# Kernel optimization log

Measured on AMD Instinct MI355X. Metric: run time of the kernel, lower is better.

The kernel has to match this reference:

```python
import jax, jax.numpy as jnp
import numpy as np

N = 16384      # nodes
E = 131072     # edges
L = 256        # latent size
H = 256        # mlp hidden size
S = 4          # message passing steps
OUT = 128      # decoder node output size
EPS = 1e-6     # flax LayerNorm epsilon


def _mlp(x, W0, b0, W1, b1):
    h = jax.nn.relu(x @ W0 + b0)
    return h @ W1 + b1


def _mlp_ln(x, W0, b0, W1, b1, ls, lb):
    y = _mlp(x, W0, b0, W1, b1)
    mu = y.mean(-1, keepdims=True)
    var = ((y - mu) ** 2).mean(-1, keepdims=True)
    return (y - mu) * jax.lax.rsqrt(var + EPS) * ls + lb


def setup_inputs() -> dict:
    key = jax.random.key(0)
    ks = iter(jax.random.split(key, 64))
    std = 0.02

    def w(shape):
        return jax.random.normal(next(ks), shape, dtype=jnp.float32) * std

    inp = {
        'node_feats': jax.random.normal(next(ks), (N, 3), dtype=jnp.float32),
        'edge_feats': jax.random.normal(next(ks), (E, 4), dtype=jnp.float32),
        'senders': jax.random.randint(next(ks), (E,), 0, N, dtype=jnp.int32),
        'receivers': jax.random.randint(next(ks), (E,), 0, N, dtype=jnp.int32),
        # node embedder MLP (3 -> H -> L) + LayerNorm
        'en_W0': w((3, H)), 'en_b0': jnp.zeros((H,)), 'en_W1': w((H, L)), 'en_b1': jnp.zeros((L,)),
        'en_ls': jnp.ones((L,)), 'en_lb': jnp.zeros((L,)),
        # edge embedder MLP (4 -> H -> L) + LayerNorm
        'ee_W0': w((4, H)), 'ee_b0': jnp.zeros((H,)), 'ee_W1': w((H, L)), 'ee_b1': jnp.zeros((L,)),
        'ee_ls': jnp.ones((L,)), 'ee_lb': jnp.zeros((L,)),
        # processor edge MLPs, stacked over S steps (3L -> H -> L) + LN
        'pe_W0': w((S, 3 * L, H)), 'pe_b0': jnp.zeros((S, H)), 'pe_W1': w((S, H, L)), 'pe_b1': jnp.zeros((S, L)),
        'pe_ls': jnp.ones((S, L)), 'pe_lb': jnp.zeros((S, L)),
        # processor node MLPs, stacked over S steps (2L -> H -> L) + LN
        'pn_W0': w((S, 2 * L, H)), 'pn_b0': jnp.zeros((S, H)), 'pn_W1': w((S, H, L)), 'pn_b1': jnp.zeros((S, L)),
        'pn_ls': jnp.ones((S, L)), 'pn_lb': jnp.zeros((S, L)),
        # node decoder MLP (L -> H -> OUT), no LayerNorm
        'dn_W0': w((L, H)), 'dn_b0': jnp.zeros((H,)), 'dn_W1': w((H, OUT)), 'dn_b1': jnp.zeros((OUT,)),
    }
    return inp


def reference(node_feats, edge_feats, senders, receivers,
              en_W0, en_b0, en_W1, en_b1, en_ls, en_lb,
              ee_W0, ee_b0, ee_W1, ee_b1, ee_ls, ee_lb,
              pe_W0, pe_b0, pe_W1, pe_b1, pe_ls, pe_lb,
              pn_W0, pn_b0, pn_W1, pn_b1, pn_ls, pn_lb,
              dn_W0, dn_b0, dn_W1, dn_b1):
    # Embed raw node/edge features into latent space.
    nodes = _mlp_ln(node_feats, en_W0, en_b0, en_W1, en_b1, en_ls, en_lb)   # [N, L]
    edges = _mlp_ln(edge_feats, ee_W0, ee_b0, ee_W1, ee_b1, ee_ls, ee_lb)   # [E, L]

    def step(carry, p):
        nodes, edges = carry
        (eW0, eb0, eW1, eb1, els, elb, nW0, nb0, nW1, nb1, nls, nlb) = p
        # Edge update: MLP on [edge, sender_node, receiver_node].
        ein = jnp.concatenate([edges, nodes[senders], nodes[receivers]], axis=-1)  # [E, 3L]
        new_e = _mlp_ln(ein, eW0, eb0, eW1, eb1, els, elb)                          # [E, L]
        # Aggregate new edge messages into receiver nodes (segment_sum).
        agg = jax.ops.segment_sum(new_e, receivers, num_segments=N)                # [N, L]
        # Node update: MLP on [node, aggregated messages].
        nin = jnp.concatenate([nodes, agg], axis=-1)                                # [N, 2L]
        new_n = _mlp_ln(nin, nW0, nb0, nW1, nb1, nls, nlb)                          # [N, L]
        # Residual connections (as in DeepTypedGraphNet processor).
        return (nodes + new_n, edges + new_e), None

    (nodes, edges), _ = jax.lax.scan(
        step, (nodes, edges),
        (pe_W0, pe_b0, pe_W1, pe_b1, pe_ls, pe_lb,
         pn_W0, pn_b0, pn_W1, pn_b1, pn_ls, pn_lb))

    # Decoder on nodes (no LayerNorm on the output head).
    out = _mlp(nodes, dn_W0, dn_b0, dn_W1, dn_b1)  # [N, OUT]
    return out
```

## Files before the change

### kernel.cpp

```cpp
#include <hip/hip_runtime.h>
#include <hip/hip_bf16.h>

#define NN 16384
#define NE 131072
#define L 256
#define SSTEPS 4
#define OUTD 128

typedef __attribute__((ext_vector_type(8))) short bf16x8;
typedef __attribute__((ext_vector_type(4))) float f32x4;

typedef const unsigned __attribute__((address_space(1)))* as1_u32p;
typedef unsigned __attribute__((address_space(3)))* as3_u32p;

__device__ __forceinline__ void gload16(const void* g, void* lds) {
  __builtin_amdgcn_global_load_lds((as1_u32p)g, (as3_u32p)lds, 16, 0, 0);
}

__device__ __forceinline__ short f2bs(float f) {
  unsigned u = __builtin_bit_cast(unsigned, f);
  u = (u + 0x7fffu + ((u >> 16) & 1u)) >> 16;
  return (short)u;
}
__device__ __forceinline__ float bs2f(short s) {
  unsigned u = ((unsigned)(unsigned short)s) << 16;
  return __builtin_bit_cast(float, u);
}
__device__ __forceinline__ unsigned cvt_pk_bf16(float lo, float hi) {
  unsigned r;
  asm("v_cvt_pk_bf16_f32 %0, %1, %2" : "=v"(r) : "v"(lo), "v"(hi));
  return r;
}
__device__ __forceinline__ bf16x8 pack_bf16x8(const float v[8]) {
  union { unsigned u[4]; bf16x8 b; } r;
#pragma unroll
  for (int k = 0; k < 4; ++k) r.u[k] = cvt_pk_bf16(v[2 * k], v[2 * k + 1]);
  return r.b;
}

__device__ __forceinline__ void store_tile(short* hs, int l, int mi, int nb,
                                           f32x4 v) {
  const int lm = l & 15, g = l >> 4;
#pragma unroll
  for (int i = 0; i < 4; ++i) {
    const float part = __shfl_xor(v[i], 1);
    if ((l & 1) == 0) {
      const int row = mi * 16 + g * 4 + i;
      const int col = nb + lm;
      const int off = (row * 512 + col * 2) ^ ((row & 7) << 4);
      *(unsigned*)((char*)hs + off) = cvt_pk_bf16(v[i], part);
    }
  }
}

template <int MI, int NT, int KC, int AST>
__device__ __forceinline__ void gemm_lds(const short* __restrict__ Wp,
                                         int Ncols, const short* hs, int n0,
                                         int l, f32x4 acc[MI][NT]) {
  const int lm = l & 15, g = l >> 4;
#pragma unroll
  for (int kc = 0; kc < KC; ++kc) {
    bf16x8 a[MI];
#pragma unroll
    for (int mi = 0; mi < MI; ++mi) {
      const int row = mi * 16 + lm;
      const int off = (row * AST + kc * 64 + g * 16) ^ ((row & 7) << 4);
      a[mi] = *(const bf16x8*)((const char*)hs + off);
    }
#pragma unroll
    for (int ni = 0; ni < NT; ++ni) {
      const int n = n0 + ni * 16 + lm;
      bf16x8 b = *(const bf16x8*)(Wp + ((size_t)kc * Ncols + n) * 32 + g * 8);
#pragma unroll
      for (int mi = 0; mi < MI; ++mi)
        acc[mi][ni] =
            __builtin_amdgcn_mfma_f32_16x16x32_bf16(a[mi], b, acc[mi][ni], 0, 0, 0);
    }
  }
}

__global__ void pack_w(const float* __restrict__ src, short* __restrict__ dst,
                       int K, int N, int cnt) {
  const size_t total = (size_t)K * N * cnt;
  for (size_t i = (size_t)blockIdx.x * blockDim.x + threadIdx.x; i < total;
       i += (size_t)gridDim.x * blockDim.x) {
    const size_t mat = i / ((size_t)K * N);
    const int rem = (int)(i - mat * (size_t)K * N);
    const int k = rem / N, n = rem - k * N;
    dst[mat * (size_t)K * N + ((size_t)(k >> 5) * N + n) * 32 + (k & 31)] =
        f2bs(src[i]);
  }
}

__global__ void pack_w0_pad(const float* __restrict__ src,
                            short* __restrict__ dst, int Kreal) {
  const int i = blockIdx.x * 256 + threadIdx.x;
  if (i >= 256 * 32) return;
  const int n = i >> 5, k = i & 31;
  dst[n * 32 + k] = (k < Kreal) ? f2bs(src[k * 256 + n]) : (short)0;
}

__device__ __forceinline__ void stage_tile256(const short* __restrict__ src0,
                                              short* As, int w, int l) {
#pragma unroll
  for (int i = 0; i < 4; ++i) {
    const int rbase = w * 8 + i * 2;
    const int r = rbase + (l >> 5);
    const int boff = ((l & 31) * 16) ^ ((r & 7) << 4);
    gload16((const char*)(src0 + (size_t)r * L) + boff, As + rbase * 256);
  }
}

__device__ __forceinline__ void stage_nodes_half16(
    const short* __restrict__ a_src, short* As, int w, int l, int n0) {
#pragma unroll
  for (int i = 0; i < 4; ++i) {
    const int r = w * 4 + i;
    if (l < 32) {
      const int cb = (l * 16) ^ ((r & 7) << 4);
      gload16((const char*)(a_src + (size_t)(n0 + r) * L) + cb, As + r * 512);
    }
  }
}

__global__ void csr_hist(const int* __restrict__ recv, int* __restrict__ deg) {
  const int e = blockIdx.x * 256 + threadIdx.x;
  atomicAdd(&deg[recv[e]], 1);
}
__global__ __launch_bounds__(256) void csr_scan(const int* __restrict__ deg,
                                                int* __restrict__ start,
                                                int* __restrict__ cursor) {
  __shared__ int part[256];
  const int t = threadIdx.x;
  int s = 0;
  for (int i = 0; i < NN / 256; ++i) s += deg[t * (NN / 256) + i];
  part[t] = s;
  __syncthreads();
  if (t == 0) {
    int acc = 0;
    for (int i = 0; i < 256; ++i) {
      const int v = part[i];
      part[i] = acc;
      acc += v;
    }
  }
  __syncthreads();
  int acc = part[t];
  for (int i = 0; i < NN / 256; ++i) {
    const int n = t * (NN / 256) + i;
    start[n] = acc;
    cursor[n] = acc;
    acc += deg[n];
  }
  if (t == 255) start[NN] = acc;
}
__global__ void csr_scatter(const int* __restrict__ recv,
                            int* __restrict__ cursor, int* __restrict__ elist) {
  const int e = blockIdx.x * 256 + threadIdx.x;
  const int p = atomicAdd(&cursor[recv[e]], 1);
  elist[p] = e;
}
__global__ void csr_sort(const int* __restrict__ start, int* __restrict__ elist) {
  const int n = blockIdx.x * blockDim.x + threadIdx.x;
  if (n >= NN) return;
  const int b = start[n], e = start[n + 1];
  for (int i = b + 1; i < e; ++i) {
    const int v = elist[i];
    int j = i - 1;
    while (j >= b && elist[j] > v) {
      elist[j + 1] = elist[j];
      --j;
    }
    elist[j + 1] = v;
  }
}
__global__ void permute_se(const int* __restrict__ elist,
                           const int* __restrict__ senders,
                           const int* __restrict__ receivers,
                           int* __restrict__ sn_p, int* __restrict__ rc_p) {
  const int p = blockIdx.x * 256 + threadIdx.x;
  const int e = elist[p];
  sn_p[p] = senders[e];
  rc_p[p] = receivers[e];
}

__device__ __forceinline__ void ln_row(const short* smem, int row, int seg,
                                       const float lsv[16], const float lbv[16],
                                       float ne[16]) {
  const int off0 = (row * 512 + seg * 16) ^ ((row & 7) << 4);
  const int off1 = (row * 512 + 256 + seg * 16) ^ ((row & 7) << 4);
  const bf16x8 y0 = *(const bf16x8*)((const char*)smem + off0);
  const bf16x8 y1 = *(const bf16x8*)((const char*)smem + off1);
  float v[16];
#pragma unroll
  for (int k = 0; k < 8; ++k) {
    v[k] = bs2f(y0[k]);
    v[8 + k] = bs2f(y1[k]);
  }
  float s = 0.f;
#pragma unroll
  for (int k = 0; k < 16; ++k) s += v[k];
#pragma unroll
  for (int o = 1; o < 16; o <<= 1) s += __shfl_xor(s, o);
  const float mu = s * (1.f / 256.f);
  float sq = 0.f;
#pragma unroll
  for (int k = 0; k < 16; ++k) {
    const float d = v[k] - mu;
    sq += d * d;
  }
#pragma unroll
  for (int o = 1; o < 16; o <<= 1) sq += __shfl_xor(sq, o);
  const float rstd = rsqrtf(sq * (1.f / 256.f) + 1e-6f);
#pragma unroll
  for (int k = 0; k < 16; ++k) ne[k] = (v[k] - mu) * rstd * lsv[k] + lbv[k];
}

__device__ __forceinline__ void load16(const float* __restrict__ p, int seg,
                                       float d[16]) {
  const float4 a0 = *(const float4*)(p + seg * 8);
  const float4 a1 = *(const float4*)(p + seg * 8 + 4);
  const float4 a2 = *(const float4*)(p + 128 + seg * 8);
  const float4 a3 = *(const float4*)(p + 128 + seg * 8 + 4);
  d[0] = a0.x; d[1] = a0.y; d[2] = a0.z; d[3] = a0.w;
  d[4] = a1.x; d[5] = a1.y; d[6] = a1.z; d[7] = a1.w;
  d[8] = a2.x; d[9] = a2.y; d[10] = a2.z; d[11] = a2.w;
  d[12] = a3.x; d[13] = a3.y; d[14] = a3.z; d[15] = a3.w;
}

__global__ __launch_bounds__(256, 4) void proj_mfma(
    const short* __restrict__ nodes_b, const short* __restrict__ Wfull,
    short* __restrict__ NSb, short* __restrict__ NRb) {
  __shared__ char smem[16384];
  short* As = (short*)smem;
  const int t = threadIdx.x, w = t >> 6, l = t & 63;
  const int tr = t >> 4, seg = t & 15;
  const int n0 = blockIdx.x * 32;
  const short* Wp = Wfull + (size_t)(8 + blockIdx.y * 8) * 256 * 32;
  short* out = blockIdx.y ? NRb : NSb;

  stage_tile256(nodes_b + (size_t)n0 * L, As, w, l);
  __syncthreads();

  f32x4 acc[2][4] = {};
  gemm_lds<2, 4, 8, 512>(Wp, L, As, w * 64, l, acc);
  __syncthreads();
#pragma unroll
  for (int ni = 0; ni < 4; ++ni)
#pragma unroll
    for (int mi = 0; mi < 2; ++mi)
      store_tile(As, l, mi, w * 64 + ni * 16, acc[mi][ni]);
  __syncthreads();

#pragma unroll
  for (int p = 0; p < 2; ++p) {
    const int row = p * 16 + tr;
    const int off0 = (row * 512 + seg * 16) ^ ((row & 7) << 4);
    const int off1 = (row * 512 + 256 + seg * 16) ^ ((row & 7) << 4);
    *(bf16x8*)(out + (size_t)(n0 + row) * L + seg * 8) =
        *(const bf16x8*)((const char*)As + off0);
    *(bf16x8*)(out + (size_t)(n0 + row) * L + 128 + seg * 8) =
        *(const bf16x8*)((const char*)As + off1);
  }
}

__global__ __launch_bounds__(256, 4) void edge_step_mfma(
    const short* __restrict__ NSb, const short* __restrict__ NRb,
    short* __restrict__ edges_b, short* __restrict__ new_e,
    const int* __restrict__ senders, const int* __restrict__ receivers,
    const short* __restrict__ W0p, const float* __restrict__ b0,
    const short* __restrict__ W1p, const float* __restrict__ b1,
    const float* __restrict__ ls, const float* __restrict__ lb) {
  __shared__ char smem[32768];
  short* As = (short*)smem;
  short* nsrB = (short*)(smem + 16384);
  const int t = threadIdx.x, w = t >> 6, l = t & 63;
  const int lm = l & 15, g = l >> 4;
  const int tr = t >> 4, seg = t & 15;
  const int e0 = blockIdx.x * 32;

  const int sn0 = senders[e0 + tr], rc0 = receivers[e0 + tr];
  const int sn1 = senders[e0 + 16 + tr], rc1 = receivers[e0 + 16 + tr];
  stage_tile256(edges_b + (size_t)e0 * L, As, w, l);
  __syncthreads();

  bf16x8 gn[2][2], gr[2][2];
  {
    const short* p0 = NSb + (size_t)sn0 * L + seg * 8;
    gn[0][0] = *(const bf16x8*)p0;
    gn[0][1] = *(const bf16x8*)(p0 + 128);
    const short* p1 = NSb + (size_t)sn1 * L + seg * 8;
    gn[1][0] = *(const bf16x8*)p1;
    gn[1][1] = *(const bf16x8*)(p1 + 128);
    const short* q0 = NRb + (size_t)rc0 * L + seg * 8;
    gr[0][0] = *(const bf16x8*)q0;
    gr[0][1] = *(const bf16x8*)(q0 + 128);
    const short* q1 = NRb + (size_t)rc1 * L + seg * 8;
    gr[1][0] = *(const bf16x8*)q1;
    gr[1][1] = *(const bf16x8*)(q1 + 128);
  }

  f32x4 acc[2][4] = {};
  gemm_lds<2, 4, 8, 512>(W0p, L, As, w * 64, l, acc);

  bf16x8 old0[2], old1[2];
#pragma unroll
  for (int p = 0; p < 2; ++p) {
    const int row = p * 16 + tr;
    old0[p] = *(const bf16x8*)((const char*)As +
                               ((row * 512 + seg * 16) ^ ((row & 7) << 4)));
    old1[p] = *(const bf16x8*)((const char*)As +
                               ((row * 512 + 256 + seg * 16) ^ ((row & 7) << 4)));
  }

#pragma unroll
  for (int p = 0; p < 2; ++p) {
    const int row = p * 16 + tr;
    float s[16];
#pragma unroll
    for (int k = 0; k < 8; ++k) {
      s[k] = bs2f(gn[p][0][k]) + bs2f(gr[p][0][k]);
      s[8 + k] = bs2f(gn[p][1][k]) + bs2f(gr[p][1][k]);
    }
    const int off0 = (row * 512 + seg * 16) ^ ((row & 7) << 4);
    const int off1 = (row * 512 + 256 + seg * 16) ^ ((row & 7) << 4);
    *(bf16x8*)((char*)nsrB + off0) = pack_bf16x8(s);
    *(bf16x8*)((char*)nsrB + off1) = pack_bf16x8(s + 8);
  }
  __syncthreads();

#pragma unroll
  for (int ni = 0; ni < 4; ++ni) {
    const float bia = b0[w * 64 + ni * 16 + lm];
    const int col = w * 64 + ni * 16 + lm;
#pragma unroll
    for (int mi = 0; mi < 2; ++mi) {
      f32x4 v = acc[mi][ni];
#pragma unroll
      for (int i = 0; i < 4; ++i) {
        const int row = mi * 16 + g * 4 + i;
        const int noff = (row * 512 + col * 2) ^ ((row & 7) << 4);
        v[i] = fmaxf(v[i] + bia + bs2f(*(const short*)((const char*)nsrB + noff)),
                     0.f);
      }
      store_tile(As, l, mi, w * 64 + ni * 16, v);
    }
  }
  __syncthreads();

  f32x4 acc2[2][4] = {};
  gemm_lds<2, 4, 8, 512>(W1p, L, As, w * 64, l, acc2);
#pragma unroll
  for (int ni = 0; ni < 4; ++ni) {
    const float bia = b1[w * 64 + ni * 16 + lm];
#pragma unroll
    for (int mi = 0; mi < 2; ++mi) {
      f32x4 v = acc2[mi][ni];
#pragma unroll
      for (int i = 0; i < 4; ++i) v[i] += bia;
      store_tile(nsrB, l, mi, w * 64 + ni * 16, v);
    }
  }
  __syncthreads();

  float lsv[16], lbv[16];
  load16(ls, seg, lsv);
  load16(lb, seg, lbv);
#pragma unroll
  for (int p = 0; p < 2; ++p) {
    const int row = p * 16 + tr;
    float ne[16];
    ln_row(nsrB, row, seg, lsv, lbv, ne);
    const size_t e = (size_t)(e0 + row);
    *(bf16x8*)(new_e + e * L + seg * 8) = pack_bf16x8(ne);
    *(bf16x8*)(new_e + e * L + 128 + seg * 8) = pack_bf16x8(ne + 8);
    float r0[8], r1[8];
#pragma unroll
    for (int k = 0; k < 8; ++k) {
      r0[k] = bs2f(old0[p][k]) + ne[k];
      r1[k] = bs2f(old1[p][k]) + ne[8 + k];
    }
    *(bf16x8*)(edges_b + e * L + seg * 8) = pack_bf16x8(r0);
    *(bf16x8*)(edges_b + e * L + 128 + seg * 8) = pack_bf16x8(r1);
  }
}

__global__ __launch_bounds__(256, 4) void node_step_mfma(
    float* __restrict__ nodes_f, short* __restrict__ nodes_b,
    const short* __restrict__ new_e, const int* __restrict__ start,
    const short* __restrict__ W0p, const float* __restrict__ b0,
    const short* __restrict__ W1p, const float* __restrict__ b1,
    const float* __restrict__ ls, const float* __restrict__ lb,
    const short* __restrict__ W0nS, const short* __restrict__ W0nR,
    short* __restrict__ NSb, short* __restrict__ NRb) {
  __shared__ char smem[16384];
  short* As = (short*)smem;
  short* hb = (short*)smem;
  short* yb = (short*)(smem + 8192);
  const int t = threadIdx.x, w = t >> 6, l = t & 63;
  const int lm = l & 15;
  const int tr = t >> 4, seg = t & 15;
  const int n0 = blockIdx.x * 16;

  stage_nodes_half16(nodes_b, As, w, l, n0);

  {
    const int grp = t >> 5, lc = t & 31;
#pragma unroll
    for (int i = 0; i < 2; ++i) {
      const int r = grp * 2 + i;
      const int n = n0 + r;
      const int b = start[n], e = start[n + 1];
      float acc[8] = {0.f, 0.f, 0.f, 0.f, 0.f, 0.f, 0.f, 0.f};
      for (int j = b; j < e; ++j) {
        const bf16x8 v = *(const bf16x8*)(new_e + (size_t)j * L + lc * 8);
#pragma unroll
        for (int k = 0; k < 8; ++k) acc[k] += bs2f(v[k]);
      }
      const int off = (r * 1024 + 512 + lc * 16) ^ ((r & 7) << 4);
      *(bf16x8*)((char*)As + off) = pack_bf16x8(acc);
    }
  }
  __syncthreads();

  f32x4 acc[1][4] = {};
  gemm_lds<1, 4, 16, 1024>(W0p, L, As, w * 64, l, acc);
  __syncthreads();

#pragma unroll
  for (int ni = 0; ni < 4; ++ni) {
    const float bia = b0[w * 64 + ni * 16 + lm];
    f32x4 v = acc[0][ni];
#pragma unroll
    for (int i = 0; i < 4; ++i) v[i] = fmaxf(v[i] + bia, 0.f);
    store_tile(hb, l, 0, w * 64 + ni * 16, v);
  }
  __syncthreads();

  f32x4 acc2[1][4] = {};
  gemm_lds<1, 4, 8, 512>(W1p, L, hb, w * 64, l, acc2);
  __syncthreads();
#pragma unroll
  for (int ni = 0; ni < 4; ++ni) {
    const float bia = b1[w * 64 + ni * 16 + lm];
    f32x4 v = acc2[0][ni];
#pragma unroll
    for (int i = 0; i < 4; ++i) v[i] += bia;
    store_tile(yb, l, 0, w * 64 + ni * 16, v);
  }
  __syncthreads();

  float lsv[16], lbv[16];
  load16(ls, seg, lsv);
  load16(lb, seg, lbv);
  {
    const int row = tr;
    float ne[16];
    ln_row(yb, row, seg, lsv, lbv, ne);
    const size_t n = (size_t)(n0 + row);
    float* nf = nodes_f + n * L;
    float fv[16];
    load16(nf, seg, fv);
    float nv[16];
#pragma unroll
    for (int k = 0; k < 16; ++k) nv[k] = fv[k] + ne[k];
    *(float4*)(nf + seg * 8) = make_float4(nv[0], nv[1], nv[2], nv[3]);
    *(float4*)(nf + seg * 8 + 4) = make_float4(nv[4], nv[5], nv[6], nv[7]);
    *(float4*)(nf + 128 + seg * 8) = make_float4(nv[8], nv[9], nv[10], nv[11]);
    *(float4*)(nf + 128 + seg * 8 + 4) = make_float4(nv[12], nv[13], nv[14], nv[15]);
    const bf16x8 nb0 = pack_bf16x8(nv);
    const bf16x8 nb1 = pack_bf16x8(nv + 8);
    *(bf16x8*)(nodes_b + n * L + seg * 8) = nb0;
    *(bf16x8*)(nodes_b + n * L + 128 + seg * 8) = nb1;
    const int off0 = (row * 512 + seg * 16) ^ ((row & 7) << 4);
    const int off1 = (row * 512 + 256 + seg * 16) ^ ((row & 7) << 4);
    *(bf16x8*)((char*)hb + off0) = nb0;
    *(bf16x8*)((char*)hb + off1) = nb1;
  }

  if (W0nS == nullptr) return;
  __syncthreads();

  {
    f32x4 pa[1][4] = {};
    gemm_lds<1, 4, 8, 512>(W0nS, L, hb, w * 64, l, pa);
#pragma unroll
    for (int ni = 0; ni < 4; ++ni)
      store_tile(yb, l, 0, w * 64 + ni * 16, pa[0][ni]);
    __syncthreads();
    {
      const int row = tr;
      const int off0 = (row * 512 + seg * 16) ^ ((row & 7) << 4);
      const int off1 = (row * 512 + 256 + seg * 16) ^ ((row & 7) << 4);
      *(bf16x8*)(NSb + (size_t)(n0 + row) * L + seg * 8) =
          *(const bf16x8*)((const char*)yb + off0);
      *(bf16x8*)(NSb + (size_t)(n0 + row) * L + 128 + seg * 8) =
          *(const bf16x8*)((const char*)yb + off1);
    }
  }
  __syncthreads();

  {
    f32x4 pa[1][4] = {};
    gemm_lds<1, 4, 8, 512>(W0nR, L, hb, w * 64, l, pa);
#pragma unroll
    for (int ni = 0; ni < 4; ++ni)
      store_tile(yb, l, 0, w * 64 + ni * 16, pa[0][ni]);
    __syncthreads();
    {
      const int row = tr;
      const int off0 = (row * 512 + seg * 16) ^ ((row & 7) << 4);
      const int off1 = (row * 512 + 256 + seg * 16) ^ ((row & 7) << 4);
      *(bf16x8*)(NRb + (size_t)(n0 + row) * L + seg * 8) =
          *(const bf16x8*)((const char*)yb + off0);
      *(bf16x8*)(NRb + (size_t)(n0 + row) * L + 128 + seg * 8) =
          *(const bf16x8*)((const char*)yb + off1);
    }
  }
}

template <int K1, bool WF32>
__global__ __launch_bounds__(256) void embed_mfma(
    const float* __restrict__ x, const int* __restrict__ gidx,
    const short* __restrict__ W0p, const float* __restrict__ b0,
    const short* __restrict__ W1p, const float* __restrict__ b1,
    const float* __restrict__ ls, const float* __restrict__ lb,
    float* __restrict__ dst_f, short* __restrict__ dst_b) {
  __shared__ short hs[64 * 256];
  __shared__ short xsb[64 * 32];
  const int t = threadIdx.x, w = t >> 6, l = t & 63;
  const int lm = l & 15, g = l >> 4;
  const int tr = t >> 4, seg = t & 15;
  const int r0 = blockIdx.x * 64;

  if (t < 64) {
    const size_t srow = gidx ? (size_t)gidx[r0 + t] : (size_t)(r0 + t);
    const float* xr = x + srow * K1;
    float v[8] = {0.f, 0.f, 0.f, 0.f, 0.f, 0.f, 0.f, 0.f};
#pragma unroll
    for (int k = 0; k < K1; ++k) v[k] = xr[k];
    bf16x8 z;
#pragma unroll
    for (int k = 0; k < 8; ++k) z[k] = 0;
    char* rb = (char*)xsb + t * 64;
    *(bf16x8*)(rb + (0 ^ ((t & 3) << 4))) = pack_bf16x8(v);
#pragma unroll
    for (int gi = 1; gi < 4; ++gi) *(bf16x8*)(rb + ((gi * 16) ^ ((t & 3) << 4))) = z;
  }
  __syncthreads();

  f32x4 acc[4][4] = {};
  {
    bf16x8 a[4];
#pragma unroll
    for (int mi = 0; mi < 4; ++mi) {
      const int row = mi * 16 + lm;
      a[mi] = *(const bf16x8*)((const char*)xsb + row * 64 +
                               ((g * 16) ^ ((row & 3) << 4)));
    }
#pragma unroll
    for (int ni = 0; ni < 4; ++ni) {
      const int n = w * 64 + ni * 16 + lm;
      bf16x8 b = *(const bf16x8*)(W0p + n * 32 + g * 8);
#pragma unroll
      for (int mi = 0; mi < 4; ++mi)
        acc[mi][ni] =
            __builtin_amdgcn_mfma_f32_16x16x32_bf16(a[mi], b, acc[mi][ni], 0, 0, 0);
    }
  }
#pragma unroll
  for (int ni = 0; ni < 4; ++ni) {
    const float bia = b0[w * 64 + ni * 16 + lm];
#pragma unroll
    for (int mi = 0; mi < 4; ++mi) {
      f32x4 v = acc[mi][ni];
#pragma unroll
      for (int i = 0; i < 4; ++i) v[i] = fmaxf(v[i] + bia, 0.f);
      store_tile(hs, l, mi, w * 64 + ni * 16, v);
    }
  }
  __syncthreads();

  f32x4 acc2[4][4] = {};
  gemm_lds<4, 4, 8, 512>(W1p, L, hs, w * 64, l, acc2);
  __syncthreads();
#pragma unroll
  for (int ni = 0; ni < 4; ++ni) {
    const float bia = b1[w * 64 + ni * 16 + lm];
#pragma unroll
    for (int mi = 0; mi < 4; ++mi) {
      f32x4 v = acc2[mi][ni];
#pragma unroll
      for (int i = 0; i < 4; ++i) v[i] += bia;
      store_tile(hs, l, mi, w * 64 + ni * 16, v);
    }
  }
  __syncthreads();

  float lsv[16], lbv[16];
  load16(ls, seg, lsv);
  load16(lb, seg, lbv);
#pragma unroll
  for (int p = 0; p < 4; ++p) {
    const int row = p * 16 + tr;
    float ne[16];
    ln_row(hs, row, seg, lsv, lbv, ne);
    const size_t n = (size_t)(r0 + row);
    *(bf16x8*)(dst_b + n * L + seg * 8) = pack_bf16x8(ne);
    *(bf16x8*)(dst_b + n * L + 128 + seg * 8) = pack_bf16x8(ne + 8);
    if (WF32) {
      float* df = dst_f + n * L;
      *(float4*)(df + seg * 8) = make_float4(ne[0], ne[1], ne[2], ne[3]);
      *(float4*)(df + seg * 8 + 4) = make_float4(ne[4], ne[5], ne[6], ne[7]);
      *(float4*)(df + 128 + seg * 8) = make_float4(ne[8], ne[9], ne[10], ne[11]);
      *(float4*)(df + 128 + seg * 8 + 4) =
          make_float4(ne[12], ne[13], ne[14], ne[15]);
    }
  }
}

__global__ __launch_bounds__(256) void decoder_mfma(
    const short* __restrict__ nodes_b, const short* __restrict__ W0p,
    const float* __restrict__ b0, const short* __restrict__ W1p,
    const float* __restrict__ b1, float* __restrict__ out) {
  __shared__ short hs[64 * 256];
  const int t = threadIdx.x, w = t >> 6, l = t & 63;
  const int lm = l & 15, g = l >> 4;
  const int n0 = blockIdx.x * 64;

  const short* baseA[4];
#pragma unroll
  for (int mi = 0; mi < 4; ++mi)
    baseA[mi] = nodes_b + (size_t)(n0 + mi * 16 + lm) * L;

  f32x4 acc[4][4] = {};
#pragma unroll
  for (int kc = 0; kc < 8; ++kc) {
    const int koff = kc * 32 + g * 8;
    bf16x8 a[4];
#pragma unroll
    for (int mi = 0; mi < 4; ++mi) a[mi] = *(const bf16x8*)(baseA[mi] + koff);
#pragma unroll
    for (int ni = 0; ni < 4; ++ni) {
      const int n = w * 64 + ni * 16 + lm;
      bf16x8 b = *(const bf16x8*)(W0p + ((size_t)kc * L + n) * 32 + g * 8);
#pragma unroll
      for (int mi = 0; mi < 4; ++mi)
        acc[mi][ni] = __builtin_amdgcn_mfma_f32_16x16x32_bf16(a[mi], b,
                                                             acc[mi][ni],
                                                             0, 0, 0);
    }
  }
#pragma unroll
  for (int ni = 0; ni < 4; ++ni) {
    const float bia = b0[w * 64 + ni * 16 + lm];
#pragma unroll
    for (int mi = 0; mi < 4; ++mi) {
      f32x4 v = acc[mi][ni];
#pragma unroll
      for (int i = 0; i < 4; ++i) v[i] = fmaxf(v[i] + bia, 0.f);
      store_tile(hs, l, mi, w * 64 + ni * 16, v);
    }
  }
  __syncthreads();

  f32x4 acc2[4][2] = {};
  gemm_lds<4, 2, 8, 512>(W1p, OUTD, hs, w * 32, l, acc2);

  float b14[2];
#pragma unroll
  for (int ni = 0; ni < 2; ++ni) b14[ni] = b1[w * 32 + ni * 16 + lm];
#pragma unroll
  for (int mi = 0; mi < 4; ++mi)
#pragma unroll
    for (int ni = 0; ni < 2; ++ni)
#pragma unroll
      for (int i = 0; i < 4; ++i) {
        const int row = n0 + mi * 16 + g * 4 + i;
        const int col = w * 32 + ni * 16 + lm;
        out[(size_t)row * OUTD + col] = acc2[mi][ni][i] + b14[ni];
      }
}

extern "C" void kernel_launch(void* const* d_in, const int* in_sizes, int n_in,
                              void* d_out, int out_size, void* d_ws,
                              size_t ws_size, hipStream_t stream) {
  const float* node_feats = (const float*)d_in[0];
  const float* edge_feats = (const float*)d_in[1];
  const int* senders = (const int*)d_in[2];
  const int* receivers = (const int*)d_in[3];
  auto f = [&](int i) { return (const float*)d_in[i]; };

  char* p = (char*)d_ws;
  auto alloc = [&](size_t bytes) {
    char* q = p;
    p += (bytes + 255) & ~(size_t)255;
    return q;
  };
  float* nodes_f = (float*)alloc((size_t)NN * L * 4);
  short* nodes_b = (short*)alloc((size_t)NN * L * 2);
  short* edges_b = (short*)alloc((size_t)NE * L * 2);
  short* new_e = (short*)alloc((size_t)NE * L * 2);
  short* NSb = (short*)alloc((size_t)NN * L * 2);
  short* NRb = (short*)alloc((size_t)NN * L * 2);
  int* deg = (int*)alloc((size_t)NN * 4);
  int* start = (int*)alloc((size_t)(NN + 16) * 4);
  int* cursor = (int*)alloc((size_t)NN * 4);
  int* elist = (int*)alloc((size_t)NE * 4);
  int* sn_p = (int*)alloc((size_t)NE * 4);
  int* rc_p = (int*)alloc((size_t)NE * 4);
  short* en_W0p = (short*)alloc(256 * 32 * 2);
  short* ee_W0p = (short*)alloc(256 * 32 * 2);
  short* en_W1p = (short*)alloc(65536 * 2);
  short* ee_W1p = (short*)alloc(65536 * 2);
  short* pe_W0p = (short*)alloc((size_t)4 * 768 * 256 * 2);
  short* pe_W1p = (short*)alloc((size_t)4 * 65536 * 2);
  short* pn_W0p = (short*)alloc((size_t)4 * 512 * 256 * 2);
  short* pn_W1p = (short*)alloc((size_t)4 * 65536 * 2);
  short* dn_W0p = (short*)alloc(65536 * 2);
  short* dn_W1p = (short*)alloc(32768 * 2);

  hipMemsetAsync(deg, 0, (size_t)NN * 4, stream);
  csr_hist<<<NE / 256, 256, 0, stream>>>(receivers, deg);
  csr_scan<<<1, 256, 0, stream>>>(deg, start, cursor);
  csr_scatter<<<NE / 256, 256, 0, stream>>>(receivers, cursor, elist);
  csr_sort<<<NN / 256, 256, 0, stream>>>(start, elist);
  permute_se<<<NE / 256, 256, 0, stream>>>(elist, senders, receivers, sn_p,
                                           rc_p);

  pack_w0_pad<<<32, 256, 0, stream>>>(f(4), en_W0p, 3);
  pack_w0_pad<<<32, 256, 0, stream>>>(f(10), ee_W0p, 4);
  pack_w<<<256, 256, 0, stream>>>(f(6), en_W1p, 256, 256, 1);
  pack_w<<<256, 256, 0, stream>>>(f(12), ee_W1p, 256, 256, 1);
  pack_w<<<1024, 256, 0, stream>>>(f(16), pe_W0p, 768, 256, 4);
  pack_w<<<512, 256, 0, stream>>>(f(18), pe_W1p, 256, 256, 4);
  pack_w<<<1024, 256, 0, stream>>>(f(22), pn_W0p, 512, 256, 4);
  pack_w<<<512, 256, 0, stream>>>(f(24), pn_W1p, 256, 256, 4);
  pack_w<<<256, 256, 0, stream>>>(f(28), dn_W0p, 256, 256, 1);
  pack_w<<<128, 256, 0, stream>>>(f(30), dn_W1p, 256, 128, 1);

  embed_mfma<3, true><<<NN / 64, 256, 0, stream>>>(
      node_feats, nullptr, en_W0p, f(5), en_W1p, f(7), f(8), f(9), nodes_f,
      nodes_b);
  embed_mfma<4, false><<<NE / 64, 256, 0, stream>>>(
      edge_feats, elist, ee_W0p, f(11), ee_W1p, f(13), f(14), f(15), nullptr,
      edges_b);

  for (int s = 0; s < SSTEPS; ++s) {
    const short* W0s = pe_W0p + (size_t)s * 768 * 256;
    if (s == 0)
      proj_mfma<<<dim3(NN / 32, 2), 256, 0, stream>>>(nodes_b, W0s, NSb, NRb);
    edge_step_mfma<<<NE / 32, 256, 0, stream>>>(
        NSb, NRb, edges_b, new_e, sn_p, rc_p, W0s, f(17) + (size_t)s * 256,
        pe_W1p + (size_t)s * 65536, f(19) + (size_t)s * 256,
        f(20) + (size_t)s * 256, f(21) + (size_t)s * 256);
    const short* W0n = (s + 1 < SSTEPS) ? pe_W0p + (size_t)(s + 1) * 768 * 256
                                        : nullptr;
    node_step_mfma<<<NN / 16, 256, 0, stream>>>(
        nodes_f, nodes_b, new_e, start, pn_W0p + (size_t)s * 512 * 256,
        f(23) + (size_t)s * 256, pn_W1p + (size_t)s * 65536,
        f(25) + (size_t)s * 256, f(26) + (size_t)s * 256,
        f(27) + (size_t)s * 256, W0n ? W0n + (size_t)8 * 256 * 32 : nullptr,
        W0n ? W0n + (size_t)16 * 256 * 32 : nullptr, NSb, NRb);
  }

  decoder_mfma<<<NN / 64, 256, 0, stream>>>(nodes_b, dn_W0p, f(29), dn_W1p,
                                            f(31), (float*)d_out);
}
```

Baseline: 806.6 us.

## Process two edge tiles per block and prefetch the next tile during the epilogue

The edge step kernel now handles 64 edges per block as two 32-edge tiles. Staging of the second tile's edges and its sender/receiver gathers is issued before the first tile's LayerNorm epilogue, so that load latency overlaps compute. A block-index swizzle also remaps which edge range each block handles. The cost is half as many blocks, which reduces parallelism across the GPU, plus an extra barrier per tile.

```diff
diff --git a/kernel.cpp b/kernel.cpp
--- a/kernel.cpp
+++ b/kernel.cpp
@@ -121,6 +121,23 @@
       gload16((const char*)(a_src + (size_t)(n0 + r) * L) + cb, As + r * 512);
     }
   }
+}
+
+__device__ __forceinline__ void issue_gathers(
+    const short* __restrict__ NSb, const short* __restrict__ NRb, int sn0,
+    int sn1, int rc0, int rc1, int seg, bf16x8 gn[2][2], bf16x8 gr[2][2]) {
+  const short* p0 = NSb + (size_t)sn0 * L + seg * 8;
+  gn[0][0] = *(const bf16x8*)p0;
+  gn[0][1] = *(const bf16x8*)(p0 + 128);
+  const short* p1 = NSb + (size_t)sn1 * L + seg * 8;
+  gn[1][0] = *(const bf16x8*)p1;
+  gn[1][1] = *(const bf16x8*)(p1 + 128);
+  const short* q0 = NRb + (size_t)rc0 * L + seg * 8;
+  gr[0][0] = *(const bf16x8*)q0;
+  gr[0][1] = *(const bf16x8*)(q0 + 128);
+  const short* q1 = NRb + (size_t)rc1 * L + seg * 8;
+  gr[1][0] = *(const bf16x8*)q1;
+  gr[1][1] = *(const bf16x8*)(q1 + 128);
 }
 
 __global__ void csr_hist(const int* __restrict__ recv, int* __restrict__ deg) {
@@ -277,111 +294,116 @@
   const int t = threadIdx.x, w = t >> 6, l = t & 63;
   const int lm = l & 15, g = l >> 4;
   const int tr = t >> 4, seg = t & 15;
-  const int e0 = blockIdx.x * 32;
-
-  const int sn0 = senders[e0 + tr], rc0 = receivers[e0 + tr];
-  const int sn1 = senders[e0 + 16 + tr], rc1 = receivers[e0 + 16 + tr];
-  stage_tile256(edges_b + (size_t)e0 * L, As, w, l);
-  __syncthreads();
-
+  const int lbid = ((blockIdx.x & 7) << 8) + (blockIdx.x >> 3);
+  const int ebase = lbid * 64;
+
+  int sn0 = senders[ebase + tr], rc0 = receivers[ebase + tr];
+  int sn1 = senders[ebase + 16 + tr], rc1 = receivers[ebase + 16 + tr];
+  stage_tile256(edges_b + (size_t)ebase * L, As, w, l);
   bf16x8 gn[2][2], gr[2][2];
-  {
-    const short* p0 = NSb + (size_t)sn0 * L + seg * 8;
-    gn[0][0] = *(const bf16x8*)p0;
-    gn[0][1] = *(const bf16x8*)(p0 + 128);
-    const short* p1 = NSb + (size_t)sn1 * L + seg * 8;
-    gn[1][0] = *(const bf16x8*)p1;
-    gn[1][1] = *(const bf16x8*)(p1 + 128);
-    const short* q0 = NRb + (size_t)rc0 * L + seg * 8;
-    gr[0][0] = *(const bf16x8*)q0;
-    gr[0][1] = *(const bf16x8*)(q0 + 128);
-    const short* q1 = NRb + (size_t)rc1 * L + seg * 8;
-    gr[1][0] = *(const bf16x8*)q1;
-    gr[1][1] = *(const bf16x8*)(q1 + 128);
-  }
-
-  f32x4 acc[2][4] = {};
-  gemm_lds<2, 4, 8, 512>(W0p, L, As, w * 64, l, acc);
-
-  bf16x8 old0[2], old1[2];
-#pragma unroll
-  for (int p = 0; p < 2; ++p) {
-    const int row = p * 16 + tr;
-    old0[p] = *(const bf16x8*)((const char*)As +
-                               ((row * 512 + seg * 16) ^ ((row & 7) << 4)));
-    old1[p] = *(const bf16x8*)((const char*)As +
-                               ((row * 512 + 256 + seg * 16) ^ ((row & 7) << 4)));
-  }
-
-#pragma unroll
-  for (int p = 0; p < 2; ++p) {
-    const int row = p * 16 + tr;
-    float s[16];
-#pragma unroll
-    for (int k = 0; k < 8; ++k) {
-      s[k] = bs2f(gn[p][0][k]) + bs2f(gr[p][0][k]);
-      s[8 + k] = bs2f(gn[p][1][k]) + bs2f(gr[p][1][k]);
-    }
-    const int off0 = (row * 512 + seg * 16) ^ ((row & 7) << 4);
-    const int off1 = (row * 512 + 256 + seg * 16) ^ ((row & 7) << 4);
-    *(bf16x8*)((char*)nsrB + off0) = pack_bf16x8(s);
-    *(bf16x8*)((char*)nsrB + off1) = pack_bf16x8(s + 8);
-  }
-  __syncthreads();
-
-#pragma unroll
-  for (int ni = 0; ni < 4; ++ni) {
-    const float bia = b0[w * 64 + ni * 16 + lm];
-    const int col = w * 64 + ni * 16 + lm;
-#pragma unroll
-    for (int mi = 0; mi < 2; ++mi) {
-      f32x4 v = acc[mi][ni];
-#pragma unroll
-      for (int i = 0; i < 4; ++i) {
-        const int row = mi * 16 + g * 4 + i;
-        const int noff = (row * 512 + col * 2) ^ ((row & 7) << 4);
-        v[i] = fmaxf(v[i] + bia + bs2f(*(const short*)((const char*)nsrB + noff)),
-                     0.f);
-      }
-      store_tile(As, l, mi, w * 64 + ni * 16, v);
-    }
-  }
-  __syncthreads();
-
-  f32x4 acc2[2][4] = {};
-  gemm_lds<2, 4, 8, 512>(W1p, L, As, w * 64, l, acc2);
-#pragma unroll
-  for (int ni = 0; ni < 4; ++ni) {
-    const float bia = b1[w * 64 + ni * 16 + lm];
-#pragma unroll
-    for (int mi = 0; mi < 2; ++mi) {
-      f32x4 v = acc2[mi][ni];
-#pragma unroll
-      for (int i = 0; i < 4; ++i) v[i] += bia;
-      store_tile(nsrB, l, mi, w * 64 + ni * 16, v);
-    }
-  }
-  __syncthreads();
+  issue_gathers(NSb, NRb, sn0, sn1, rc0, rc1, seg, gn, gr);
 
   float lsv[16], lbv[16];
   load16(ls, seg, lsv);
   load16(lb, seg, lbv);
-#pragma unroll
-  for (int p = 0; p < 2; ++p) {
-    const int row = p * 16 + tr;
-    float ne[16];
-    ln_row(nsrB, row, seg, lsv, lbv, ne);
-    const size_t e = (size_t)(e0 + row);
-    *(bf16x8*)(new_e + e * L + seg * 8) = pack_bf16x8(ne);
-    *(bf16x8*)(new_e + e * L + 128 + seg * 8) = pack_bf16x8(ne + 8);
-    float r0[8], r1[8];
-#pragma unroll
-    for (int k = 0; k < 8; ++k) {
-      r0[k] = bs2f(old0[p][k]) + ne[k];
-      r1[k] = bs2f(old1[p][k]) + ne[8 + k];
-    }
-    *(bf16x8*)(edges_b + e * L + seg * 8) = pack_bf16x8(r0);
-    *(bf16x8*)(edges_b + e * L + 128 + seg * 8) = pack_bf16x8(r1);
+  __syncthreads();
+
+#pragma unroll
+  for (int tt = 0; tt < 2; ++tt) {
+    const int e0 = ebase + tt * 32;
+
+    f32x4 acc[2][4] = {};
+    gemm_lds<2, 4, 8, 512>(W0p, L, As, w * 64, l, acc);
+
+    bf16x8 old0[2], old1[2];
+#pragma unroll
+    for (int p = 0; p < 2; ++p) {
+      const int row = p * 16 + tr;
+      old0[p] = *(const bf16x8*)((const char*)As +
+                                 ((row * 512 + seg * 16) ^ ((row & 7) << 4)));
+      old1[p] = *(const bf16x8*)((const char*)As + ((row * 512 + 256 +
+                                                     seg * 16) ^
+                                                    ((row & 7) << 4)));
+    }
+
+#pragma unroll
+    for (int p = 0; p < 2; ++p) {
+      const int row = p * 16 + tr;
+      float s[16];
+#pragma unroll
+      for (int k = 0; k < 8; ++k) {
+        s[k] = bs2f(gn[p][0][k]) + bs2f(gr[p][0][k]);
+        s[8 + k] = bs2f(gn[p][1][k]) + bs2f(gr[p][1][k]);
+      }
+      const int off0 = (row * 512 + seg * 16) ^ ((row & 7) << 4);
+      const int off1 = (row * 512 + 256 + seg * 16) ^ ((row & 7) << 4);
+      *(bf16x8*)((char*)nsrB + off0) = pack_bf16x8(s);
+      *(bf16x8*)((char*)nsrB + off1) = pack_bf16x8(s + 8);
+    }
+    __syncthreads();
+
+#pragma unroll
+    for (int ni = 0; ni < 4; ++ni) {
+      const float bia = b0[w * 64 + ni * 16 + lm];
+      const int col = w * 64 + ni * 16 + lm;
+#pragma unroll
+      for (int mi = 0; mi < 2; ++mi) {
+        f32x4 v = acc[mi][ni];
+#pragma unroll
+        for (int i = 0; i < 4; ++i) {
+          const int row = mi * 16 + g * 4 + i;
+          const int noff = (row * 512 + col * 2) ^ ((row & 7) << 4);
+          v[i] = fmaxf(
+              v[i] + bia + bs2f(*(const short*)((const char*)nsrB + noff)),
+              0.f);
+        }
+        store_tile(As, l, mi, w * 64 + ni * 16, v);
+      }
+    }
+    __syncthreads();
+
+    f32x4 acc2[2][4] = {};
+    gemm_lds<2, 4, 8, 512>(W1p, L, As, w * 64, l, acc2);
+#pragma unroll
+    for (int ni = 0; ni < 4; ++ni) {
+      const float bia = b1[w * 64 + ni * 16 + lm];
+#pragma unroll
+      for (int mi = 0; mi < 2; ++mi) {
+        f32x4 v = acc2[mi][ni];
+#pragma unroll
+        for (int i = 0; i < 4; ++i) v[i] += bia;
+        store_tile(nsrB, l, mi, w * 64 + ni * 16, v);
+      }
+    }
+    __syncthreads();
+
+    if (tt == 0) {
+      sn0 = senders[ebase + 32 + tr];
+      rc0 = receivers[ebase + 32 + tr];
+      sn1 = senders[ebase + 48 + tr];
+      rc1 = receivers[ebase + 48 + tr];
+      stage_tile256(edges_b + (size_t)(ebase + 32) * L, As, w, l);
+      issue_gathers(NSb, NRb, sn0, sn1, rc0, rc1, seg, gn, gr);
+    }
+
+#pragma unroll
+    for (int p = 0; p < 2; ++p) {
+      const int row = p * 16 + tr;
+      float ne[16];
+      ln_row(nsrB, row, seg, lsv, lbv, ne);
+      const size_t e = (size_t)(e0 + row);
+      *(bf16x8*)(new_e + e * L + seg * 8) = pack_bf16x8(ne);
+      *(bf16x8*)(new_e + e * L + 128 + seg * 8) = pack_bf16x8(ne + 8);
+      float r0[8], r1[8];
+#pragma unroll
+      for (int k = 0; k < 8; ++k) {
+        r0[k] = bs2f(old0[p][k]) + ne[k];
+        r1[k] = bs2f(old1[p][k]) + ne[8 + k];
+      }
+      *(bf16x8*)(edges_b + e * L + seg * 8) = pack_bf16x8(r0);
+      *(bf16x8*)(edges_b + e * L + 128 + seg * 8) = pack_bf16x8(r1);
+    }
+    __syncthreads();
   }
 }
 
@@ -750,7 +772,7 @@
     const short* W0s = pe_W0p + (size_t)s * 768 * 256;
     if (s == 0)
       proj_mfma<<<dim3(NN / 32, 2), 256, 0, stream>>>(nodes_b, W0s, NSb, NRb);
-    edge_step_mfma<<<NE / 32, 256, 0, stream>>>(
+    edge_step_mfma<<<NE / 64, 256, 0, stream>>>(
         NSb, NRb, edges_b, new_e, sn_p, rc_p, W0s, f(17) + (size_t)s * 256,
         pe_W1p + (size_t)s * 65536, f(19) + (size_t)s * 256,
         f(20) + (size_t)s * 256, f(21) + (size_t)s * 256);
```

After: 1.792 ms. 2.22x slower.
